# Optimization experiments

Measured on AMD Instinct MI355X. Metric: run time of the kernel, lower is better.

The kernel has to match this reference:

```python
import jax, jax.numpy as jnp
import numpy as np

N_NODES = 100000
N_EDGES = 1600000
IN_F = 128
HID_F = 128
OUT_F = 128

def _glorot(key, shape):
    lim = np.sqrt(6.0 / (shape[0] + shape[1]))
    return jax.random.uniform(key, shape, jnp.float32, -lim, lim)

def setup_inputs() -> dict:
    key = jax.random.key(0)
    ks = jax.random.split(key, 9)
    x = jax.random.normal(ks[0], (N_NODES, IN_F), jnp.float32)
    src = jax.random.randint(ks[1], (N_EDGES,), 0, N_NODES, jnp.int32)
    dst = jax.random.randint(ks[2], (N_EDGES,), 0, N_NODES, jnp.int32)
    return {
        'x': x, 'src': src, 'dst': dst,
        'W_self1': _glorot(ks[3], (IN_F, HID_F)),
        'W_neigh1': _glorot(ks[4], (IN_F, HID_F)),
        'b1': jnp.zeros((HID_F,), jnp.float32),
        'W_self2': _glorot(ks[5], (HID_F, OUT_F)),
        'W_neigh2': _glorot(ks[6], (HID_F, OUT_F)),
        'b2': jnp.zeros((OUT_F,), jnp.float32),
    }

def _sage_mean(h, src, dst, W_self, W_neigh, b, n_nodes):
    # mean-aggregate src features onto dst (DGL SAGEConv 'mean')
    msg_sum = jax.ops.segment_sum(h[src], dst, num_segments=n_nodes)  # [N, d]
    deg = jax.ops.segment_sum(jnp.ones_like(dst, jnp.float32), dst, num_segments=n_nodes)
    h_neigh = msg_sum / jnp.maximum(deg, 1.0)[:, None]
    return h @ W_self + h_neigh @ W_neigh + b

def reference(x, src, dst, W_self1, W_neigh1, b1, W_self2, W_neigh2, b2):
    n = x.shape[0]
    h = _sage_mean(x, src, dst, W_self1, W_neigh1, b1, n)
    h = _sage_mean(h, src, dst, W_self2, W_neigh2, b2, n)
    # edge-wise dot product score between endpoint features (u_dot_v)
    s = jnp.sum(h[src] * h[dst], axis=-1)  # [E]
    smin, smax = jnp.min(s), jnp.max(s)
    return (s - smin) / (smax - smin)
```

## Files before the change

kernel.cpp:

```cpp
#include <hip/hip_runtime.h>
#include <hip/hip_bf16.h>

#define F 128

typedef unsigned int uint;
typedef unsigned short ushort;
typedef __attribute__((ext_vector_type(8))) short short8;
typedef __attribute__((ext_vector_type(4))) float f32x4;

__device__ inline ushort f2bf(float f) {
    uint u = __float_as_uint(f);
    u += 0x7FFF + ((u >> 16) & 1);
    return (ushort)(u >> 16);
}
__device__ inline float2 bf2f(uint u) {
    return make_float2(__uint_as_float(u << 16), __uint_as_float(u & 0xFFFF0000u));
}

__global__ __launch_bounds__(256) void rank_kernel(const int* __restrict__ dst,
                                                   int* __restrict__ cnt,
                                                   ushort* __restrict__ rel, int E) {
    int e = blockIdx.x * 256 + threadIdx.x;
    if (e < E) rel[e] = (ushort)atomicAdd(&cnt[dst[e]], 1);
}

__global__ __launch_bounds__(256) void scan_block(const int* __restrict__ cnt,
                                                  int* __restrict__ off,
                                                  int* __restrict__ bsum, int N) {
    __shared__ int t[256];
    int i = blockIdx.x * 256 + threadIdx.x;
    int v = (i < N) ? cnt[i] : 0;
    t[threadIdx.x] = v;
    __syncthreads();
    for (int o = 1; o < 256; o <<= 1) {
        int x = (threadIdx.x >= o) ? t[threadIdx.x - o] : 0;
        __syncthreads();
        t[threadIdx.x] += x;
        __syncthreads();
    }
    if (i < N) off[i] = t[threadIdx.x] - v;
    if (threadIdx.x == 255) bsum[blockIdx.x] = t[255];
}

__global__ __launch_bounds__(512) void scan_sums(int* __restrict__ bsum, int nb) {
    __shared__ int t[512];
    int v = (threadIdx.x < nb) ? bsum[threadIdx.x] : 0;
    t[threadIdx.x] = v;
    __syncthreads();
    for (int o = 1; o < 512; o <<= 1) {
        int x = (threadIdx.x >= o) ? t[threadIdx.x - o] : 0;
        __syncthreads();
        t[threadIdx.x] += x;
        __syncthreads();
    }
    if (threadIdx.x < nb) bsum[threadIdx.x] = t[threadIdx.x] - v;
}

__global__ __launch_bounds__(256) void scan_add_rdeg(int* __restrict__ off,
                                                     const int* __restrict__ bsum,
                                                     const int* __restrict__ cnt,
                                                     float* __restrict__ rdeg, int N) {
    int i = blockIdx.x * 256 + threadIdx.x;
    if (i >= N) return;
    off[i] += bsum[blockIdx.x];
    rdeg[i] = 1.0f / fmaxf((float)cnt[i], 1.0f);
}

__global__ __launch_bounds__(256) void fill_kernel(const int* __restrict__ src,
                                                   const int* __restrict__ dst,
                                                   const int* __restrict__ off,
                                                   const ushort* __restrict__ rel,
                                                   int* __restrict__ srcS,
                                                   int* __restrict__ rank, int E) {
    int e = blockIdx.x * 256 + threadIdx.x;
    if (e >= E) return;
    int p = off[dst[e]] + (int)rel[e];
    srcS[p] = src[e];
    rank[e] = p;
}

__global__ __launch_bounds__(256) void wprep(const float* __restrict__ W0,
                                             const float* __restrict__ W1,
                                             const float* __restrict__ W2,
                                             const float* __restrict__ W3,
                                             ushort* __restrict__ Wt) {
    int idx = blockIdx.x * 256 + threadIdx.x;
    if (idx >= 4 * 16384) return;
    int mat = idx >> 14;
    int pos = idx & 16383;
    int k = pos >> 7, n = pos & 127;
    const float* W = (mat == 0) ? W0 : (mat == 1) ? W1 : (mat == 2) ? W2 : W3;
    Wt[mat * 16384 + n * 128 + k] = f2bf(W[k * 128 + n]);
}

__global__ __launch_bounds__(256) void cast_bf16(const float* __restrict__ in,
                                                 uint* __restrict__ outb, int n4) {
    int i = blockIdx.x * 256 + threadIdx.x;
    if (i >= n4) return;
    float4 v = ((const float4*)in)[i];
    uint ua = (uint)f2bf(v.x) | ((uint)f2bf(v.y) << 16);
    uint ub = (uint)f2bf(v.z) | ((uint)f2bf(v.w) << 16);
    ((uint2*)outb)[i] = make_uint2(ua, ub);
}

__global__ __launch_bounds__(256) void agg_gather(const uint* __restrict__ hb,
                                                  const int* __restrict__ off,
                                                  const int* __restrict__ srcS,
                                                  const float* __restrict__ rdeg,
                                                  uint* __restrict__ msgb, int N, int E) {
    int node = blockIdx.x * 4 + (threadIdx.x >> 6);
    int lane = threadIdx.x & 63;
    if (node >= N) return;
    int p = off[node];
    int pe = (node == N - 1) ? E : off[node + 1];
    float2 acc = make_float2(0.f, 0.f);
    for (; p + 7 < pe; p += 8) {
        int s0 = srcS[p],     s1 = srcS[p + 1], s2 = srcS[p + 2], s3 = srcS[p + 3];
        int s4 = srcS[p + 4], s5 = srcS[p + 5], s6 = srcS[p + 6], s7 = srcS[p + 7];
        float2 f0 = bf2f(hb[(size_t)s0 * 64 + lane]);
        float2 f1 = bf2f(hb[(size_t)s1 * 64 + lane]);
        float2 f2 = bf2f(hb[(size_t)s2 * 64 + lane]);
        float2 f3 = bf2f(hb[(size_t)s3 * 64 + lane]);
        float2 f4 = bf2f(hb[(size_t)s4 * 64 + lane]);
        float2 f5 = bf2f(hb[(size_t)s5 * 64 + lane]);
        float2 f6 = bf2f(hb[(size_t)s6 * 64 + lane]);
        float2 f7 = bf2f(hb[(size_t)s7 * 64 + lane]);
        acc.x += ((f0.x + f1.x) + (f2.x + f3.x)) + ((f4.x + f5.x) + (f6.x + f7.x));
        acc.y += ((f0.y + f1.y) + (f2.y + f3.y)) + ((f4.y + f5.y) + (f6.y + f7.y));
    }
    for (; p < pe; ++p) {
        float2 f = bf2f(hb[(size_t)srcS[p] * 64 + lane]);
        acc.x += f.x;
        acc.y += f.y;
    }
    float rd = rdeg[node];
    msgb[(size_t)node * 64 + lane] = (uint)f2bf(acc.x * rd) | ((uint)f2bf(acc.y * rd) << 16);
}

__global__ __launch_bounds__(256) void sage_mfma(const uint* __restrict__ hb,
                                                 const uint* __restrict__ mb,
                                                 const uint* __restrict__ Wt,
                                                 const float* __restrict__ bias,
                                                 ushort* __restrict__ outb, int N) {
    int wave = threadIdx.x >> 6, lane = threadIdx.x & 63;
    int m = lane & 15, q = lane >> 4;
    int r0 = blockIdx.x * 64 + wave * 16;
    int arow = r0 + m;
    if (arow >= N) arow = N - 1;

    f32x4 acc[8];
#pragma unroll
    for (int t = 0; t < 8; t++) acc[t] = (f32x4){0.f, 0.f, 0.f, 0.f};

    const uint* hrow = hb + (size_t)arow * 64;
    const uint* mrow = mb + (size_t)arow * 64;
#pragma unroll
    for (int sel = 0; sel < 2; sel++) {
        const uint* arowp = sel ? mrow : hrow;
        const uint* wsel = Wt + sel * 8192;
#pragma unroll
        for (int kk = 0; kk < 4; kk++) {
            int ko = kk * 16 + q * 4;
            short8 a = *(const short8*)(arowp + ko);
#pragma unroll
            for (int t = 0; t < 8; t++) {
                short8 b = *(const short8*)(wsel + (size_t)(16 * t + m) * 64 + ko);
                acc[t] = __builtin_amdgcn_mfma_f32_16x16x32_bf16(a, b, acc[t], 0, 0, 0);
            }
        }
    }

#pragma unroll
    for (int t = 0; t < 8; t++) {
        float bs = bias[16 * t + m];
#pragma unroll
        for (int r = 0; r < 4; r++) {
            int orow = r0 + q * 4 + r;
            if (orow < N) outb[(size_t)orow * 128 + 16 * t + m] = f2bf(acc[t][r] + bs);
        }
    }
}

__global__ __launch_bounds__(256) void edge_score_csr(const uint* __restrict__ hb,
                                                      const int* __restrict__ off,
                                                      const int* __restrict__ srcS,
                                                      float* __restrict__ sc,
                                                      float2* __restrict__ pmm, int N, int E) {
    int node = blockIdx.x * 4 + (threadIdx.x >> 6);
    int lane = threadIdx.x & 63;
    float lmin = INFINITY, lmax = -INFINITY;

    if (node < N) {
        int p = off[node];
        int pe = (node == N - 1) ? E : off[node + 1];
        if (p < pe) {
            float2 d = bf2f(hb[(size_t)node * 64 + lane]);
            for (; p + 7 < pe; p += 8) {
                int s0 = srcS[p],     s1 = srcS[p + 1], s2 = srcS[p + 2], s3 = srcS[p + 3];
                int s4 = srcS[p + 4], s5 = srcS[p + 5], s6 = srcS[p + 6], s7 = srcS[p + 7];
                float2 a0 = bf2f(hb[(size_t)s0 * 64 + lane]);
                float2 a1 = bf2f(hb[(size_t)s1 * 64 + lane]);
                float2 a2 = bf2f(hb[(size_t)s2 * 64 + lane]);
                float2 a3 = bf2f(hb[(size_t)s3 * 64 + lane]);
                float2 a4 = bf2f(hb[(size_t)s4 * 64 + lane]);
                float2 a5 = bf2f(hb[(size_t)s5 * 64 + lane]);
                float2 a6 = bf2f(hb[(size_t)s6 * 64 + lane]);
                float2 a7 = bf2f(hb[(size_t)s7 * 64 + lane]);
                float v0 = a0.x * d.x + a0.y * d.y;
                float v1 = a1.x * d.x + a1.y * d.y;
                float v2 = a2.x * d.x + a2.y * d.y;
                float v3 = a3.x * d.x + a3.y * d.y;
                float v4 = a4.x * d.x + a4.y * d.y;
                float v5 = a5.x * d.x + a5.y * d.y;
                float v6 = a6.x * d.x + a6.y * d.y;
                float v7 = a7.x * d.x + a7.y * d.y;
#pragma unroll
                for (int o = 32; o > 0; o >>= 1) {
                    v0 += __shfl_down(v0, o);
                    v1 += __shfl_down(v1, o);
                    v2 += __shfl_down(v2, o);
                    v3 += __shfl_down(v3, o);
                    v4 += __shfl_down(v4, o);
                    v5 += __shfl_down(v5, o);
                    v6 += __shfl_down(v6, o);
                    v7 += __shfl_down(v7, o);
                }
                if (lane == 0) {
                    sc[p] = v0; sc[p + 1] = v1; sc[p + 2] = v2; sc[p + 3] = v3;
                    sc[p + 4] = v4; sc[p + 5] = v5; sc[p + 6] = v6; sc[p + 7] = v7;
                    float mn = fminf(fminf(fminf(v0, v1), fminf(v2, v3)),
                                     fminf(fminf(v4, v5), fminf(v6, v7)));
                    float mx = fmaxf(fmaxf(fmaxf(v0, v1), fmaxf(v2, v3)),
                                     fmaxf(fmaxf(v4, v5), fmaxf(v6, v7)));
                    lmin = fminf(lmin, mn);
                    lmax = fmaxf(lmax, mx);
                }
            }
            for (; p < pe; ++p) {
                float2 a = bf2f(hb[(size_t)srcS[p] * 64 + lane]);
                float v = a.x * d.x + a.y * d.y;
#pragma unroll
                for (int o = 32; o > 0; o >>= 1) v += __shfl_down(v, o);
                if (lane == 0) {
                    sc[p] = v;
                    lmin = fminf(lmin, v);
                    lmax = fmaxf(lmax, v);
                }
            }
        }
    }

#pragma unroll
    for (int o = 1; o <= 32; o <<= 1) {
        lmin = fminf(lmin, __shfl_xor(lmin, o));
        lmax = fmaxf(lmax, __shfl_xor(lmax, o));
    }
    __shared__ float smin[4], smax[4];
    int wv = threadIdx.x >> 6;
    if (lane == 0) { smin[wv] = lmin; smax[wv] = lmax; }
    __syncthreads();
    if (threadIdx.x == 0) {
        float m = fminf(fminf(smin[0], smin[1]), fminf(smin[2], smin[3]));
        float M = fmaxf(fmaxf(smax[0], smax[1]), fmaxf(smax[2], smax[3]));
        pmm[blockIdx.x] = make_float2(m, M);
    }
}

__global__ __launch_bounds__(1024) void minmax_final(const float2* __restrict__ pmm,
                                                     float* __restrict__ mmf, int nb) {
    float vmin = INFINITY, vmax = -INFINITY;
    for (int i = threadIdx.x; i < nb; i += 1024) {
        float2 v = pmm[i];
        vmin = fminf(vmin, v.x);
        vmax = fmaxf(vmax, v.y);
    }
#pragma unroll
    for (int o = 1; o <= 32; o <<= 1) {
        vmin = fminf(vmin, __shfl_xor(vmin, o));
        vmax = fmaxf(vmax, __shfl_xor(vmax, o));
    }
    __shared__ float smin[16], smax[16];
    int lane = threadIdx.x & 63, wv = threadIdx.x >> 6;
    if (lane == 0) { smin[wv] = vmin; smax[wv] = vmax; }
    __syncthreads();
    if (threadIdx.x == 0) {
        float m = smin[0], M = smax[0];
        for (int w = 1; w < 16; w++) { m = fminf(m, smin[w]); M = fmaxf(M, smax[w]); }
        mmf[0] = m;
        mmf[1] = M;
    }
}

__global__ __launch_bounds__(256) void norm_kernel(const float* __restrict__ sc,
                                                   const int* __restrict__ rank,
                                                   float* __restrict__ out,
                                                   const float* __restrict__ mmf, int E) {
    float mn = mmf[0];
    float mx = mmf[1];
    float inv = 1.0f / (mx - mn);
    int i = blockIdx.x * 256 + threadIdx.x;
    if (i < E) out[i] = (sc[rank[i]] - mn) * inv;
}

extern "C" void kernel_launch(void* const* d_in, const int* in_sizes, int n_in,
                              void* d_out, int out_size, void* d_ws, size_t ws_size,
                              hipStream_t stream) {
    const float* x   = (const float*)d_in[0];
    const int*   src = (const int*)d_in[1];
    const int*   dst = (const int*)d_in[2];
    const float* Ws1 = (const float*)d_in[3];
    const float* Wn1 = (const float*)d_in[4];
    const float* b1  = (const float*)d_in[5];
    const float* Ws2 = (const float*)d_in[6];
    const float* Wn2 = (const float*)d_in[7];
    const float* b2  = (const float*)d_in[8];

    int N = in_sizes[0] / F;
    int E = in_sizes[1];
    float* out = (float*)d_out;

    int nbN = (N + 255) / 256;
    int nbE = (E + 255) / 256;
    int nbEdgeBlocks = (N + 3) / 4;
    int NF4 = N * F / 4;

    int* off  = (int*)d_ws;
    int* cnt  = off + N;
    int* srcS = cnt + N;
    int* rank = srcS + E;
    int* relsc = rank + E;
    ushort* rel = (ushort*)relsc;
    float* sc   = (float*)relsc;
    int* bsum = relsc + E;
    float* rdeg = (float*)(bsum + 1024);
    float* mmf = (float*)(rdeg + N);
    float2* pmm = (float2*)(mmf + 4);
    uint* Wtb = (uint*)(pmm + 25600);
    size_t elemOff = 3 * (size_t)N + 3 * (size_t)E + 1024 + 4 + 51200 + 32768;
    elemOff = (elemOff + 3) & ~(size_t)3;
    uint* xb   = (uint*)d_ws + elemOff;
    uint* msgb = xb + (size_t)N * 64;
    uint* h1b  = msgb + (size_t)N * 64;
    uint* h2b  = h1b + (size_t)N * 64;

    hipMemsetAsync(cnt, 0, (size_t)N * sizeof(int), stream);

    rank_kernel<<<nbE, 256, 0, stream>>>(dst, cnt, rel, E);
    scan_block<<<nbN, 256, 0, stream>>>(cnt, off, bsum, N);
    scan_sums<<<1, 512, 0, stream>>>(bsum, nbN);
    scan_add_rdeg<<<nbN, 256, 0, stream>>>(off, bsum, cnt, rdeg, N);
    fill_kernel<<<nbE, 256, 0, stream>>>(src, dst, off, rel, srcS, rank, E);

    wprep<<<256, 256, 0, stream>>>(Ws1, Wn1, Ws2, Wn2, (ushort*)Wtb);
    cast_bf16<<<(NF4 + 255) / 256, 256, 0, stream>>>(x, xb, NF4);

    agg_gather<<<(N + 3) / 4, 256, 0, stream>>>(xb, off, srcS, rdeg, msgb, N, E);
    sage_mfma<<<(N + 63) / 64, 256, 0, stream>>>(xb, msgb, Wtb, b1, (ushort*)h1b, N);

    agg_gather<<<(N + 3) / 4, 256, 0, stream>>>(h1b, off, srcS, rdeg, msgb, N, E);
    sage_mfma<<<(N + 63) / 64, 256, 0, stream>>>(h1b, msgb, Wtb + 16384, b2, (ushort*)h2b, N);

    edge_score_csr<<<nbEdgeBlocks, 256, 0, stream>>>(h2b, off, srcS, sc, pmm, N, E);
    minmax_final<<<1, 1024, 0, stream>>>(pmm, mmf, nbEdgeBlocks);
    norm_kernel<<<(E + 255) / 256, 256, 0, stream>>>(sc, rank, out, mmf, E);
}
```

Before: 677.9 us.

## Compute edge dot-product scores with MFMA over 16-edge tiles

Replaces the per-edge wave-wide shuffle reduction in the edge-score kernel with a bf16 16x16x32 MFMA. Each lane of a wave loads a 16-byte slice of one of 16 source rows, and the destination node's row is broadcast as the B operand. This removes the shuffle-reduction chains and issues wider, more numerous concurrent gathers per iteration. Tail edges are handled by clamping the index and masking the writes, which wastes some MFMA lanes and loads on low-degree nodes.

```diff
diff --git a/kernel.cpp b/kernel.cpp
--- a/kernel.cpp
+++ b/kernel.cpp
@@ -181,70 +181,54 @@
     }
 }
 
-__global__ __launch_bounds__(256) void edge_score_csr(const uint* __restrict__ hb,
-                                                      const int* __restrict__ off,
-                                                      const int* __restrict__ srcS,
-                                                      float* __restrict__ sc,
-                                                      float2* __restrict__ pmm, int N, int E) {
+__global__ __launch_bounds__(256) void edge_score_mfma(const uint* __restrict__ hb,
+                                                       const int* __restrict__ off,
+                                                       const int* __restrict__ srcS,
+                                                       float* __restrict__ sc,
+                                                       float2* __restrict__ pmm, int N, int E) {
     int node = blockIdx.x * 4 + (threadIdx.x >> 6);
     int lane = threadIdx.x & 63;
+    int m = lane & 15, q = lane >> 4;
     float lmin = INFINITY, lmax = -INFINITY;
 
     if (node < N) {
         int p = off[node];
         int pe = (node == N - 1) ? E : off[node + 1];
         if (p < pe) {
-            float2 d = bf2f(hb[(size_t)node * 64 + lane]);
-            for (; p + 7 < pe; p += 8) {
-                int s0 = srcS[p],     s1 = srcS[p + 1], s2 = srcS[p + 2], s3 = srcS[p + 3];
-                int s4 = srcS[p + 4], s5 = srcS[p + 5], s6 = srcS[p + 6], s7 = srcS[p + 7];
-                float2 a0 = bf2f(hb[(size_t)s0 * 64 + lane]);
-                float2 a1 = bf2f(hb[(size_t)s1 * 64 + lane]);
-                float2 a2 = bf2f(hb[(size_t)s2 * 64 + lane]);
-                float2 a3 = bf2f(hb[(size_t)s3 * 64 + lane]);
-                float2 a4 = bf2f(hb[(size_t)s4 * 64 + lane]);
-                float2 a5 = bf2f(hb[(size_t)s5 * 64 + lane]);
-                float2 a6 = bf2f(hb[(size_t)s6 * 64 + lane]);
-                float2 a7 = bf2f(hb[(size_t)s7 * 64 + lane]);
-                float v0 = a0.x * d.x + a0.y * d.y;
-                float v1 = a1.x * d.x + a1.y * d.y;
-                float v2 = a2.x * d.x + a2.y * d.y;
-                float v3 = a3.x * d.x + a3.y * d.y;
-                float v4 = a4.x * d.x + a4.y * d.y;
-                float v5 = a5.x * d.x + a5.y * d.y;
-                float v6 = a6.x * d.x + a6.y * d.y;
-                float v7 = a7.x * d.x + a7.y * d.y;
-#pragma unroll
-                for (int o = 32; o > 0; o >>= 1) {
-                    v0 += __shfl_down(v0, o);
-                    v1 += __shfl_down(v1, o);
-                    v2 += __shfl_down(v2, o);
-                    v3 += __shfl_down(v3, o);
-                    v4 += __shfl_down(v4, o);
-                    v5 += __shfl_down(v5, o);
-                    v6 += __shfl_down(v6, o);
-                    v7 += __shfl_down(v7, o);
+            const uint* nrow = hb + (size_t)node * 64;
+            short8 bfr[4];
+#pragma unroll
+            for (int kk = 0; kk < 4; kk++)
+                bfr[kk] = *(const short8*)(nrow + kk * 16 + q * 4);
+
+            for (; p < pe; p += 16) {
+                int idx = p + m;
+                if (idx >= pe) idx = pe - 1;
+                const uint* arow = hb + (size_t)srcS[idx] * 64;
+                f32x4 acc = (f32x4){0.f, 0.f, 0.f, 0.f};
+#pragma unroll
+                for (int kk = 0; kk < 4; kk++) {
+                    short8 a = *(const short8*)(arow + kk * 16 + q * 4);
+                    acc = __builtin_amdgcn_mfma_f32_16x16x32_bf16(a, bfr[kk], acc, 0, 0, 0);
                 }
-                if (lane == 0) {
-                    sc[p] = v0; sc[p + 1] = v1; sc[p + 2] = v2; sc[p + 3] = v3;
-                    sc[p + 4] = v4; sc[p + 5] = v5; sc[p + 6] = v6; sc[p + 7] = v7;
-                    float mn = fminf(fminf(fminf(v0, v1), fminf(v2, v3)),
-                                     fminf(fminf(v4, v5), fminf(v6, v7)));
-                    float mx = fmaxf(fmaxf(fmaxf(v0, v1), fmaxf(v2, v3)),
-                                     fmaxf(fmaxf(v4, v5), fmaxf(v6, v7)));
-                    lmin = fminf(lmin, mn);
-                    lmax = fmaxf(lmax, mx);
-                }
-            }
-            for (; p < pe; ++p) {
-                float2 a = bf2f(hb[(size_t)srcS[p] * 64 + lane]);
-                float v = a.x * d.x + a.y * d.y;
-#pragma unroll
-                for (int o = 32; o > 0; o >>= 1) v += __shfl_down(v, o);
-                if (lane == 0) {
-                    sc[p] = v;
-                    lmin = fminf(lmin, v);
-                    lmax = fmaxf(lmax, v);
+                if (m == 0) {
+                    if (p + 16 <= pe) {
+                        *(float4*)(sc + p + q * 4) = make_float4(acc[0], acc[1], acc[2], acc[3]);
+                        float mn = fminf(fminf(acc[0], acc[1]), fminf(acc[2], acc[3]));
+                        float mx = fmaxf(fmaxf(acc[0], acc[1]), fmaxf(acc[2], acc[3]));
+                        lmin = fminf(lmin, mn);
+                        lmax = fmaxf(lmax, mx);
+                    } else {
+#pragma unroll
+                        for (int r = 0; r < 4; r++) {
+                            int e = p + q * 4 + r;
+                            if (e < pe) {
+                                sc[e] = acc[r];
+                                lmin = fminf(lmin, acc[r]);
+                                lmax = fmaxf(lmax, acc[r]);
+                            }
+                        }
+                    }
                 }
             }
         }
@@ -260,9 +244,9 @@
     if (lane == 0) { smin[wv] = lmin; smax[wv] = lmax; }
     __syncthreads();
     if (threadIdx.x == 0) {
-        float m = fminf(fminf(smin[0], smin[1]), fminf(smin[2], smin[3]));
-        float M = fmaxf(fmaxf(smax[0], smax[1]), fmaxf(smax[2], smax[3]));
-        pmm[blockIdx.x] = make_float2(m, M);
+        float mA = fminf(fminf(smin[0], smin[1]), fminf(smin[2], smin[3]));
+        float MA = fmaxf(fmaxf(smax[0], smax[1]), fmaxf(smax[2], smax[3]));
+        pmm[blockIdx.x] = make_float2(mA, MA);
     }
 }
 
@@ -360,7 +344,7 @@
     agg_gather<<<(N + 3) / 4, 256, 0, stream>>>(h1b, off, srcS, rdeg, msgb, N, E);
     sage_mfma<<<(N + 63) / 64, 256, 0, stream>>>(h1b, msgb, Wtb + 16384, b2, (ushort*)h2b, N);
 
-    edge_score_csr<<<nbEdgeBlocks, 256, 0, stream>>>(h2b, off, srcS, sc, pmm, N, E);
+    edge_score_mfma<<<nbEdgeBlocks, 256, 0, stream>>>(h2b, off, srcS, sc, pmm, N, E);
     minmax_final<<<1, 1024, 0, stream>>>(pmm, mmf, nbEdgeBlocks);
     norm_kernel<<<(E + 255) / 256, 256, 0, stream>>>(sc, rank, out, mmf, E);
 }
```

After: 616.5 us. 1.1x faster.
